# Optimization experiments

Hardware: AMD Instinct MI355X
Metric: run time of the kernel (lower is better)

## Reference

```python
import jax, jax.numpy as jnp
import numpy as np


def setup_inputs() -> dict:
    key = jax.random.key(0)
    ks = jax.random.split(key, 5)
    N, D, H, E = 8192, 1024, 4096, 8
    s = 0.02
    return {
        "x": jax.random.normal(ks[0], (N, D), jnp.float32),
        "Wr": jax.random.normal(ks[1], (D, E), jnp.float32) * s,
        "br": jnp.zeros((E,), jnp.float32),
        "W1": jax.random.normal(ks[2], (E, D, H), jnp.float32) * s,
        "b1": jnp.zeros((E, H), jnp.float32),
        "W2": jax.random.normal(ks[3], (E, H, D), jnp.float32) * s,
        "b2": jnp.zeros((E, D), jnp.float32),
        "k": 2,
    }


def reference(x, Wr, br, W1, b1, W2, b2, k):
    # Router (eval mode: no gate noise)
    logits = x @ Wr + br                      # [N, E]
    scores = jax.nn.softmax(logits, axis=-1)  # [N, E]
    topk_vals, topk_inds = jax.lax.top_k(scores, k)  # [N, k]
    N, E = scores.shape
    # dispatch_mask: zeros scattered with top-k probabilities
    dispatch_mask = jnp.zeros_like(scores).at[
        jnp.arange(N)[:, None], topk_inds
    ].set(topk_vals)                          # [N, E]
    # Dense all-expert FFN compute (faithful to the original wasteful pattern)
    h = jax.nn.relu(jnp.einsum('nd,edh->neh', x, W1) + b1)   # [N, E, H]
    expert_outputs = jnp.einsum('neh,ehd->ned', h, W2) + b2  # [N, E, D]
    output = jnp.einsum('ned,ne->nd', expert_outputs, dispatch_mask)  # [N, D]
    # Load-balancing aux loss (torch.var is unbiased, ddof=1)
    importance = dispatch_mask.sum(axis=0)    # [E]
    imp_mean = jnp.mean(importance)
    imp_var = jnp.var(importance, ddof=1)
    aux_loss = imp_var / (imp_mean ** 2 + 1e-9)
    return output, aux_loss
```

## Files before the change

### kernel.cpp

```cpp
#include <hip/hip_runtime.h>
#include <hip/hip_bf16.h>


#define NTOK 8192
#define DDIM 1024
#define HDIM 4096
#define NEXP 8
#define NASSIGN (NTOK * 2)
#define MAX_MT 72

typedef __bf16 bf16_t;
typedef __bf16 bf16x8 __attribute__((ext_vector_type(8)));
typedef float f32x4 __attribute__((ext_vector_type(4)));

#define GLOAD16(gptr, lptr)                                                    \
  __builtin_amdgcn_global_load_lds(                                            \
      (const __attribute__((address_space(1))) void*)(gptr),                   \
      (__attribute__((address_space(3))) void*)(lptr), 16, 0, 0)


__global__ void __launch_bounds__(256) cvt_x_kernel(
    const float* __restrict__ in, bf16_t* __restrict__ out) {
  const int i = (blockIdx.x * 256 + threadIdx.x) * 8;
  const float4 a = *(const float4*)(in + i);
  const float4 b = *(const float4*)(in + i + 4);
  bf16x8 o;
  o[0] = (bf16_t)a.x; o[1] = (bf16_t)a.y; o[2] = (bf16_t)a.z; o[3] = (bf16_t)a.w;
  o[4] = (bf16_t)b.x; o[5] = (bf16_t)b.y; o[6] = (bf16_t)b.z; o[7] = (bf16_t)b.w;
  *(bf16x8*)(out + i) = o;
}

__global__ void __launch_bounds__(256) transpose_cvt_kernel(
    const float* __restrict__ in, bf16_t* __restrict__ out, int R, int C) {
  __shared__ float tile[32][33];
  const size_t mat = (size_t)R * C;
  const float* ip = in + (size_t)blockIdx.z * mat;
  bf16_t* op = out + (size_t)blockIdx.z * mat;
  const int c0 = blockIdx.x * 32, r0 = blockIdx.y * 32;
  const int tx = threadIdx.x, ty = threadIdx.y;
#pragma unroll
  for (int i = 0; i < 4; ++i) {
    const int r = ty + 8 * i;
    tile[r][tx] = ip[(size_t)(r0 + r) * C + (c0 + tx)];
  }
  __syncthreads();
#pragma unroll
  for (int i = 0; i < 4; ++i) {
    const int r = ty + 8 * i;
    op[(size_t)(c0 + r) * R + (r0 + tx)] = (bf16_t)tile[tx][r];
  }
}


__global__ void __launch_bounds__(256) router_kernel(
    const float* __restrict__ x, const float* __restrict__ Wr,
    const float* __restrict__ br, int2* __restrict__ ids,
    float2* __restrict__ prs, int* __restrict__ counts) {
  const int n = blockIdx.x;
  const int t = threadIdx.x;
  const float* xr = x + (size_t)n * DDIM;
  float acc[NEXP];
#pragma unroll
  for (int e = 0; e < NEXP; ++e) acc[e] = 0.f;
#pragma unroll
  for (int j = 0; j < DDIM / 256; ++j) {
    const int d = t + 256 * j;
    const float xv = xr[d];
    const float* w = Wr + (size_t)d * NEXP;
#pragma unroll
    for (int e = 0; e < NEXP; ++e) acc[e] += xv * w[e];
  }
  __shared__ float red[256][NEXP];
#pragma unroll
  for (int e = 0; e < NEXP; ++e) red[t][e] = acc[e];
  __syncthreads();
  for (int s = 128; s >= 1; s >>= 1) {
    if (t < s) {
#pragma unroll
      for (int e = 0; e < NEXP; ++e) red[t][e] += red[t + s][e];
    }
    __syncthreads();
  }
  if (t == 0) {
    float l[NEXP];
#pragma unroll
    for (int e = 0; e < NEXP; ++e) l[e] = red[0][e] + br[e];
    int i1 = 0; float v1 = l[0];
    for (int e = 1; e < NEXP; ++e)
      if (l[e] > v1) { v1 = l[e]; i1 = e; }
    int i2 = (i1 == 0) ? 1 : 0; float v2 = l[i2];
    for (int e = 0; e < NEXP; ++e)
      if (e != i1 && l[e] > v2) { v2 = l[e]; i2 = e; }
    float denom = 0.f;
    for (int e = 0; e < NEXP; ++e) denom += expf(l[e] - v1);
    const float p1 = expf(v1 - v1) / denom;
    const float p2 = expf(v2 - v1) / denom;
    ids[n] = make_int2(i1, i2);
    prs[n] = make_float2(p1, p2);
    atomicAdd(&counts[i1], 1);
    atomicAdd(&counts[i2], 1);
  }
}

__global__ void __launch_bounds__(256) scan_aux_kernel(
    const int* __restrict__ counts, int* __restrict__ offsets,
    int* __restrict__ tmap, const int2* __restrict__ ids,
    const float2* __restrict__ prs, float* __restrict__ aux_out) {
  const int t = threadIdx.x;
  if (t == 0) {
    int off = 0, nt = 0;
    for (int e = 0; e < NEXP; ++e) {
      offsets[e] = off;
      const int c = counts[e];
      for (int m0 = 0; m0 < c; m0 += 256) {
        tmap[nt] = e;
        tmap[MAX_MT + nt] = m0;
        ++nt;
      }
      off += c;
    }
    offsets[NEXP] = off;
    tmap[2 * MAX_MT] = nt;
  }
  float imp[NEXP];
#pragma unroll
  for (int e = 0; e < NEXP; ++e) imp[e] = 0.f;
  for (int n = t; n < NTOK; n += 256) {
    const int2 id = ids[n];
    const float2 pr = prs[n];
#pragma unroll
    for (int e = 0; e < NEXP; ++e)
      imp[e] += (id.x == e ? pr.x : 0.f) + (id.y == e ? pr.y : 0.f);
  }
  __shared__ float red[256][NEXP];
#pragma unroll
  for (int e = 0; e < NEXP; ++e) red[t][e] = imp[e];
  __syncthreads();
  for (int s = 128; s >= 1; s >>= 1) {
    if (t < s) {
#pragma unroll
      for (int e = 0; e < NEXP; ++e) red[t][e] += red[t + s][e];
    }
    __syncthreads();
  }
  if (t == 0) {
    float m = 0.f;
    for (int e = 0; e < NEXP; ++e) m += red[0][e];
    m *= (1.f / NEXP);
    float v = 0.f;
    for (int e = 0; e < NEXP; ++e) {
      const float d = red[0][e] - m;
      v += d * d;
    }
    v *= (1.f / (NEXP - 1));
    aux_out[0] = v / (m * m + 1e-9f);
  }
}

__global__ void __launch_bounds__(256) scatter_kernel(
    const int2* __restrict__ ids, const float2* __restrict__ prs,
    const int* __restrict__ offsets, int* __restrict__ cursor,
    int* __restrict__ btok, float* __restrict__ bprob) {
  const int n = blockIdx.x * 256 + threadIdx.x;
  if (n >= NTOK) return;
  const int2 id = ids[n];
  const float2 pr = prs[n];
  int p = atomicAdd(&cursor[id.x], 1);
  btok[offsets[id.x] + p] = n;
  bprob[offsets[id.x] + p] = pr.x;
  p = atomicAdd(&cursor[id.y], 1);
  btok[offsets[id.y] + p] = n;
  bprob[offsets[id.y] + p] = pr.y;
}


__global__ void __launch_bounds__(512, 2) gemm1_kernel(
    const bf16_t* __restrict__ xb, const bf16_t* __restrict__ W1t,
    const float* __restrict__ b1, const int* __restrict__ btok,
    const int* __restrict__ offsets, const int* __restrict__ counts,
    const int* __restrict__ tmap, bf16_t* __restrict__ h) {
  const int tidx = blockIdx.y;
  if (tidx >= tmap[2 * MAX_MT]) return;
  const int e = tmap[tidx];
  const int m0 = tmap[MAX_MT + tidx];
  const int cnt = counts[e];
  const int aoff = offsets[e];
  const int n0 = blockIdx.x * 256;

  __shared__ __align__(16) bf16_t Al[256 * 32];
  __shared__ __align__(16) bf16_t Bl[256 * 32];

  const int tid = threadIdx.x;
  const int wave = tid >> 6;
  const int lane = tid & 63;

  const bf16_t* asrc[2];
  const bf16_t* bsrc[2];
#pragma unroll
  for (int j = 0; j < 2; ++j) {
    const int c = j * 512 + tid;
    const int r = c >> 2;
    const int kc = (c & 3) * 8;
    int arow = m0 + r;
    if (arow > cnt - 1) arow = cnt - 1;
    const int tok = btok[aoff + arow];
    asrc[j] = xb + (size_t)tok * DDIM + kc;
    bsrc[j] = W1t + ((size_t)e * HDIM + n0 + r) * DDIM + kc;
  }
  char* AlB = (char*)Al + wave * 1024;
  char* BlB = (char*)Bl + wave * 1024;

  f32x4 acc[8][4];
#pragma unroll
  for (int mf = 0; mf < 8; ++mf)
#pragma unroll
    for (int nf = 0; nf < 4; ++nf) acc[mf][nf] = (f32x4){0.f, 0.f, 0.f, 0.f};

  const int wr = (wave >> 2) * 128;
  const int wc = (wave & 3) * 64;
  const int lrow = lane & 15;
  const int lk = (lane >> 4) * 8;

  for (int k0 = 0; k0 < DDIM; k0 += 32) {
    GLOAD16(asrc[0] + k0, AlB);
    GLOAD16(asrc[1] + k0, AlB + 8192);
    GLOAD16(bsrc[0] + k0, BlB);
    GLOAD16(bsrc[1] + k0, BlB + 8192);
    __syncthreads();
    bf16x8 af[8], bfr[4];
#pragma unroll
    for (int mf = 0; mf < 8; ++mf)
      af[mf] = *(const bf16x8*)&Al[(wr + mf * 16 + lrow) * 32 + lk];
#pragma unroll
    for (int nf = 0; nf < 4; ++nf)
      bfr[nf] = *(const bf16x8*)&Bl[(wc + nf * 16 + lrow) * 32 + lk];
#pragma unroll
    for (int mf = 0; mf < 8; ++mf)
#pragma unroll
      for (int nf = 0; nf < 4; ++nf)
        acc[mf][nf] = __builtin_amdgcn_mfma_f32_16x16x32_bf16(
            af[mf], bfr[nf], acc[mf][nf], 0, 0, 0);
    __syncthreads();
  }

  const int rbase = (lane >> 4) * 4;
  const float* b1e = b1 + (size_t)e * HDIM + n0;
#pragma unroll
  for (int nf = 0; nf < 4; ++nf) {
    const int cl = wc + nf * 16 + lrow;
    const float bb = b1e[cl];
#pragma unroll
    for (int mf = 0; mf < 8; ++mf) {
#pragma unroll
      for (int r = 0; r < 4; ++r) {
        const int grow = wr + mf * 16 + rbase + r;
        if (m0 + grow < cnt)
          h[(size_t)(aoff + m0 + grow) * HDIM + (n0 + cl)] =
              (bf16_t)fmaxf(acc[mf][nf][r] + bb, 0.f);
      }
    }
  }
}

__global__ void __launch_bounds__(512, 2) gemm2_kernel(
    const bf16_t* __restrict__ h, const bf16_t* __restrict__ W2t,
    const float* __restrict__ b2, const int* __restrict__ btok,
    const float* __restrict__ bprob, const int* __restrict__ offsets,
    const int* __restrict__ counts, const int* __restrict__ tmap,
    float* __restrict__ out) {
  const int tidx = blockIdx.y;
  if (tidx >= tmap[2 * MAX_MT]) return;
  const int e = tmap[tidx];
  const int m0 = tmap[MAX_MT + tidx];
  const int cnt = counts[e];
  const int aoff = offsets[e];
  const int n0 = blockIdx.x * 256;

  __shared__ __align__(16) bf16_t Al[256 * 32];
  __shared__ __align__(16) bf16_t Bl[256 * 32];

  const int tid = threadIdx.x;
  const int wave = tid >> 6;
  const int lane = tid & 63;

  const bf16_t* asrc[2];
  const bf16_t* bsrc[2];
#pragma unroll
  for (int j = 0; j < 2; ++j) {
    const int c = j * 512 + tid;
    const int r = c >> 2;
    const int kc = (c & 3) * 8;
    int arow = m0 + r;
    if (arow > cnt - 1) arow = cnt - 1;
    asrc[j] = h + (size_t)(aoff + arow) * HDIM + kc;
    bsrc[j] = W2t + ((size_t)e * DDIM + n0 + r) * HDIM + kc;
  }
  char* AlB = (char*)Al + wave * 1024;
  char* BlB = (char*)Bl + wave * 1024;

  f32x4 acc[8][4];
#pragma unroll
  for (int mf = 0; mf < 8; ++mf)
#pragma unroll
    for (int nf = 0; nf < 4; ++nf) acc[mf][nf] = (f32x4){0.f, 0.f, 0.f, 0.f};

  const int wr = (wave >> 2) * 128;
  const int wc = (wave & 3) * 64;
  const int lrow = lane & 15;
  const int lk = (lane >> 4) * 8;

  for (int k0 = 0; k0 < HDIM; k0 += 32) {
    GLOAD16(asrc[0] + k0, AlB);
    GLOAD16(asrc[1] + k0, AlB + 8192);
    GLOAD16(bsrc[0] + k0, BlB);
    GLOAD16(bsrc[1] + k0, BlB + 8192);
    __syncthreads();
    bf16x8 af[8], bfr[4];
#pragma unroll
    for (int mf = 0; mf < 8; ++mf)
      af[mf] = *(const bf16x8*)&Al[(wr + mf * 16 + lrow) * 32 + lk];
#pragma unroll
    for (int nf = 0; nf < 4; ++nf)
      bfr[nf] = *(const bf16x8*)&Bl[(wc + nf * 16 + lrow) * 32 + lk];
#pragma unroll
    for (int mf = 0; mf < 8; ++mf)
#pragma unroll
      for (int nf = 0; nf < 4; ++nf)
        acc[mf][nf] = __builtin_amdgcn_mfma_f32_16x16x32_bf16(
            af[mf], bfr[nf], acc[mf][nf], 0, 0, 0);
    __syncthreads();
  }

  const int rbase = (lane >> 4) * 4;
  const float* b2e = b2 + (size_t)e * DDIM + n0;
  float bb[4];
#pragma unroll
  for (int nf = 0; nf < 4; ++nf) bb[nf] = b2e[wc + nf * 16 + lrow];
#pragma unroll
  for (int mf = 0; mf < 8; ++mf) {
#pragma unroll
    for (int r = 0; r < 4; ++r) {
      const int grow = wr + mf * 16 + rbase + r;
      if (m0 + grow < cnt) {
        const int assign = aoff + m0 + grow;
        const int tok = btok[assign];
        const float p = bprob[assign];
        float* orow = out + (size_t)tok * DDIM + n0;
#pragma unroll
        for (int nf = 0; nf < 4; ++nf) {
          const int cl = wc + nf * 16 + lrow;
          atomicAdd(&orow[cl], (acc[mf][nf][r] + bb[nf]) * p);
        }
      }
    }
  }
}


extern "C" void kernel_launch(void* const* d_in, const int* in_sizes, int n_in,
                              void* d_out, int out_size, void* d_ws,
                              size_t ws_size, hipStream_t stream) {
  const float* x = (const float*)d_in[0];
  const float* Wr = (const float*)d_in[1];
  const float* br = (const float*)d_in[2];
  const float* W1 = (const float*)d_in[3];
  const float* b1 = (const float*)d_in[4];
  const float* W2 = (const float*)d_in[5];
  const float* b2 = (const float*)d_in[6];

  char* w = (char*)d_ws;
  auto alloc = [&](size_t bytes) -> char* {
    char* p = w;
    w += (bytes + 255) & ~(size_t)255;
    return p;
  };
  bf16_t* xb = (bf16_t*)alloc((size_t)NTOK * DDIM * 2);
  bf16_t* W1t = (bf16_t*)alloc((size_t)NEXP * DDIM * HDIM * 2);
  bf16_t* W2t = (bf16_t*)alloc((size_t)NEXP * DDIM * HDIM * 2);
  bf16_t* hbuf = (bf16_t*)alloc((size_t)NASSIGN * HDIM * 2);
  int* btok = (int*)alloc(NASSIGN * 4);
  float* bprob = (float*)alloc(NASSIGN * 4);
  int2* ids = (int2*)alloc(NTOK * 8);
  float2* prs = (float2*)alloc(NTOK * 8);
  int* ctrl = (int*)alloc(64);
  int* offsets = (int*)alloc(64);
  int* tmap = (int*)alloc((2 * MAX_MT + 1) * 4);
  int* counts = ctrl;
  int* cursor = ctrl + 8;
  (void)in_sizes; (void)n_in; (void)ws_size;

  float* out = (float*)d_out;

  hipMemsetAsync(d_out, 0, (size_t)out_size * 4, stream);
  hipMemsetAsync(ctrl, 0, 64, stream);

  cvt_x_kernel<<<NTOK * DDIM / 2048, 256, 0, stream>>>(x, xb);
  transpose_cvt_kernel<<<dim3(HDIM / 32, DDIM / 32, NEXP), dim3(32, 8), 0,
                         stream>>>(W1, W1t, DDIM, HDIM);
  transpose_cvt_kernel<<<dim3(DDIM / 32, HDIM / 32, NEXP), dim3(32, 8), 0,
                         stream>>>(W2, W2t, HDIM, DDIM);
  router_kernel<<<NTOK, 256, 0, stream>>>(x, Wr, br, ids, prs, counts);
  scan_aux_kernel<<<1, 256, 0, stream>>>(counts, offsets, tmap, ids, prs,
                                         out + (size_t)NTOK * DDIM);
  scatter_kernel<<<NTOK / 256, 256, 0, stream>>>(ids, prs, offsets, cursor,
                                                 btok, bprob);
  gemm1_kernel<<<dim3(HDIM / 256, MAX_MT, 1), 512, 0, stream>>>(
      xb, W1t, b1, btok, offsets, counts, tmap, hbuf);
  gemm2_kernel<<<dim3(DDIM / 256, MAX_MT, 1), 512, 0, stream>>>(
      hbuf, W2t, b2, btok, bprob, offsets, counts, tmap, out);
}
```

Baseline: 1.020 ms.

## Double-buffer expert GEMMs with BK=64, split-K gemm2, fuse x conversion into router

Both expert GEMM kernels now load 64-wide K tiles into two LDS buffers. The next tile is prefetched with global_load_lds while the current one feeds the MFMAs, and s_setprio raises priority around the MFMA section. gemm2 is split into 4 K-chunks over the grid so far more blocks run; it relies on the existing atomicAdd epilogue, with the bias added only by the first chunk. The separate x→bf16 conversion kernel is folded into the router, which already reads x. The cost is 128KB of LDS per block, which probably allows only one block per CU despite the launch bounds, plus 4× more atomic traffic into the output.

```diff
diff --git a/kernel.cpp b/kernel.cpp
--- a/kernel.cpp
+++ b/kernel.cpp
@@ -8,8 +8,10 @@
 #define NEXP 8
 #define NASSIGN (NTOK * 2)
 #define MAX_MT 72
+#define KSPLIT 4
 
 typedef __bf16 bf16_t;
+typedef __bf16 bf16x4 __attribute__((ext_vector_type(4)));
 typedef __bf16 bf16x8 __attribute__((ext_vector_type(8)));
 typedef float f32x4 __attribute__((ext_vector_type(4)));
 
@@ -18,17 +20,6 @@
       (const __attribute__((address_space(1))) void*)(gptr),                   \
       (__attribute__((address_space(3))) void*)(lptr), 16, 0, 0)
 
-
-__global__ void __launch_bounds__(256) cvt_x_kernel(
-    const float* __restrict__ in, bf16_t* __restrict__ out) {
-  const int i = (blockIdx.x * 256 + threadIdx.x) * 8;
-  const float4 a = *(const float4*)(in + i);
-  const float4 b = *(const float4*)(in + i + 4);
-  bf16x8 o;
-  o[0] = (bf16_t)a.x; o[1] = (bf16_t)a.y; o[2] = (bf16_t)a.z; o[3] = (bf16_t)a.w;
-  o[4] = (bf16_t)b.x; o[5] = (bf16_t)b.y; o[6] = (bf16_t)b.z; o[7] = (bf16_t)b.w;
-  *(bf16x8*)(out + i) = o;
-}
 
 __global__ void __launch_bounds__(256) transpose_cvt_kernel(
     const float* __restrict__ in, bf16_t* __restrict__ out, int R, int C) {
@@ -55,20 +46,25 @@
 __global__ void __launch_bounds__(256) router_kernel(
     const float* __restrict__ x, const float* __restrict__ Wr,
     const float* __restrict__ br, int2* __restrict__ ids,
-    float2* __restrict__ prs, int* __restrict__ counts) {
+    float2* __restrict__ prs, int* __restrict__ counts,
+    bf16_t* __restrict__ xb) {
   const int n = blockIdx.x;
   const int t = threadIdx.x;
-  const float* xr = x + (size_t)n * DDIM;
+  const float4 xv = ((const float4*)(x + (size_t)n * DDIM))[t];
+  bf16x4 o;
+  o[0] = (bf16_t)xv.x; o[1] = (bf16_t)xv.y;
+  o[2] = (bf16_t)xv.z; o[3] = (bf16_t)xv.w;
+  ((bf16x4*)(xb + (size_t)n * DDIM))[t] = o;
+
   float acc[NEXP];
 #pragma unroll
   for (int e = 0; e < NEXP; ++e) acc[e] = 0.f;
-#pragma unroll
-  for (int j = 0; j < DDIM / 256; ++j) {
-    const int d = t + 256 * j;
-    const float xv = xr[d];
-    const float* w = Wr + (size_t)d * NEXP;
-#pragma unroll
-    for (int e = 0; e < NEXP; ++e) acc[e] += xv * w[e];
+  const float xq[4] = {xv.x, xv.y, xv.z, xv.w};
+#pragma unroll
+  for (int q = 0; q < 4; ++q) {
+    const float* w = Wr + (size_t)(4 * t + q) * NEXP;
+#pragma unroll
+    for (int e = 0; e < NEXP; ++e) acc[e] += xq[q] * w[e];
   }
   __shared__ float red[256][NEXP];
 #pragma unroll
@@ -93,7 +89,7 @@
       if (e != i1 && l[e] > v2) { v2 = l[e]; i2 = e; }
     float denom = 0.f;
     for (int e = 0; e < NEXP; ++e) denom += expf(l[e] - v1);
-    const float p1 = expf(v1 - v1) / denom;
+    const float p1 = 1.f / denom;
     const float p2 = expf(v2 - v1) / denom;
     ids[n] = make_int2(i1, i2);
     prs[n] = make_float2(p1, p2);
@@ -187,28 +183,25 @@
   const int aoff = offsets[e];
   const int n0 = blockIdx.x * 256;
 
-  __shared__ __align__(16) bf16_t Al[256 * 32];
-  __shared__ __align__(16) bf16_t Bl[256 * 32];
+  __shared__ __align__(16) bf16_t Al[2][256 * 64];
+  __shared__ __align__(16) bf16_t Bl[2][256 * 64];
 
   const int tid = threadIdx.x;
   const int wave = tid >> 6;
   const int lane = tid & 63;
 
-  const bf16_t* asrc[2];
-  const bf16_t* bsrc[2];
-#pragma unroll
-  for (int j = 0; j < 2; ++j) {
+  const bf16_t* asrc[4];
+  const bf16_t* bsrc[4];
+#pragma unroll
+  for (int j = 0; j < 4; ++j) {
     const int c = j * 512 + tid;
-    const int r = c >> 2;
-    const int kc = (c & 3) * 8;
+    const int r = c >> 3;
+    const int kc = (c & 7) * 8;
     int arow = m0 + r;
     if (arow > cnt - 1) arow = cnt - 1;
-    const int tok = btok[aoff + arow];
-    asrc[j] = xb + (size_t)tok * DDIM + kc;
+    asrc[j] = xb + (size_t)btok[aoff + arow] * DDIM + kc;
     bsrc[j] = W1t + ((size_t)e * HDIM + n0 + r) * DDIM + kc;
   }
-  char* AlB = (char*)Al + wave * 1024;
-  char* BlB = (char*)Bl + wave * 1024;
 
   f32x4 acc[8][4];
 #pragma unroll
@@ -219,27 +212,50 @@
   const int wr = (wave >> 2) * 128;
   const int wc = (wave & 3) * 64;
   const int lrow = lane & 15;
-  const int lk = (lane >> 4) * 8;
-
-  for (int k0 = 0; k0 < DDIM; k0 += 32) {
-    GLOAD16(asrc[0] + k0, AlB);
-    GLOAD16(asrc[1] + k0, AlB + 8192);
-    GLOAD16(bsrc[0] + k0, BlB);
-    GLOAD16(bsrc[1] + k0, BlB + 8192);
-    __syncthreads();
-    bf16x8 af[8], bfr[4];
-#pragma unroll
-    for (int mf = 0; mf < 8; ++mf)
-      af[mf] = *(const bf16x8*)&Al[(wr + mf * 16 + lrow) * 32 + lk];
-#pragma unroll
-    for (int nf = 0; nf < 4; ++nf)
-      bfr[nf] = *(const bf16x8*)&Bl[(wc + nf * 16 + lrow) * 32 + lk];
-#pragma unroll
-    for (int mf = 0; mf < 8; ++mf)
+  const int lk8 = (lane >> 4) * 8;
+
+  auto stage = [&](int b, int t) {
+    const int ko = t * 64;
+    char* Ab = (char*)&Al[b][0] + wave * 1024;
+    char* Bb = (char*)&Bl[b][0] + wave * 1024;
+#pragma unroll
+    for (int j = 0; j < 4; ++j) {
+      GLOAD16(asrc[j] + ko, Ab + j * 8192);
+      GLOAD16(bsrc[j] + ko, Bb + j * 8192);
+    }
+  };
+  auto compute = [&](int b) {
+    const bf16_t* Ab = &Al[b][0];
+    const bf16_t* Bb = &Bl[b][0];
+    __builtin_amdgcn_s_setprio(1);
+#pragma unroll
+    for (int ks = 0; ks < 2; ++ks) {
+      bf16x8 af[8], bfr[4];
+#pragma unroll
+      for (int mf = 0; mf < 8; ++mf)
+        af[mf] = *(const bf16x8*)&Ab[(wr + mf * 16 + lrow) * 64 + ks * 32 + lk8];
 #pragma unroll
       for (int nf = 0; nf < 4; ++nf)
-        acc[mf][nf] = __builtin_amdgcn_mfma_f32_16x16x32_bf16(
-            af[mf], bfr[nf], acc[mf][nf], 0, 0, 0);
+        bfr[nf] = *(const bf16x8*)&Bb[(wc + nf * 16 + lrow) * 64 + ks * 32 + lk8];
+#pragma unroll
+      for (int mf = 0; mf < 8; ++mf)
+#pragma unroll
+        for (int nf = 0; nf < 4; ++nf)
+          acc[mf][nf] = __builtin_amdgcn_mfma_f32_16x16x32_bf16(
+              af[mf], bfr[nf], acc[mf][nf], 0, 0, 0);
+    }
+    __builtin_amdgcn_s_setprio(0);
+  };
+
+  stage(0, 0);
+  __syncthreads();
+#pragma unroll
+  for (int t = 0; t < 16; t += 2) {
+    stage(1, t + 1);
+    compute(0);
+    __syncthreads();
+    if (t + 2 < 16) stage(0, t + 2);
+    compute(1);
     __syncthreads();
   }
 
@@ -268,7 +284,8 @@
     const float* __restrict__ bprob, const int* __restrict__ offsets,
     const int* __restrict__ counts, const int* __restrict__ tmap,
     float* __restrict__ out) {
-  const int tidx = blockIdx.y;
+  const int tidx = blockIdx.y >> 2;
+  const int kch = blockIdx.y & 3;
   if (tidx >= tmap[2 * MAX_MT]) return;
   const int e = tmap[tidx];
   const int m0 = tmap[MAX_MT + tidx];
@@ -276,27 +293,25 @@
   const int aoff = offsets[e];
   const int n0 = blockIdx.x * 256;
 
-  __shared__ __align__(16) bf16_t Al[256 * 32];
-  __shared__ __align__(16) bf16_t Bl[256 * 32];
+  __shared__ __align__(16) bf16_t Al[2][256 * 64];
+  __shared__ __align__(16) bf16_t Bl[2][256 * 64];
 
   const int tid = threadIdx.x;
   const int wave = tid >> 6;
   const int lane = tid & 63;
 
-  const bf16_t* asrc[2];
-  const bf16_t* bsrc[2];
-#pragma unroll
-  for (int j = 0; j < 2; ++j) {
+  const bf16_t* asrc[4];
+  const bf16_t* bsrc[4];
+#pragma unroll
+  for (int j = 0; j < 4; ++j) {
     const int c = j * 512 + tid;
-    const int r = c >> 2;
-    const int kc = (c & 3) * 8;
+    const int r = c >> 3;
+    const int kc = (c & 7) * 8 + kch * 1024;
     int arow = m0 + r;
     if (arow > cnt - 1) arow = cnt - 1;
     asrc[j] = h + (size_t)(aoff + arow) * HDIM + kc;
     bsrc[j] = W2t + ((size_t)e * DDIM + n0 + r) * HDIM + kc;
   }
-  char* AlB = (char*)Al + wave * 1024;
-  char* BlB = (char*)Bl + wave * 1024;
 
   f32x4 acc[8][4];
 #pragma unroll
@@ -307,27 +322,50 @@
   const int wr = (wave >> 2) * 128;
   const int wc = (wave & 3) * 64;
   const int lrow = lane & 15;
-  const int lk = (lane >> 4) * 8;
-
-  for (int k0 = 0; k0 < HDIM; k0 += 32) {
-    GLOAD16(asrc[0] + k0, AlB);
-    GLOAD16(asrc[1] + k0, AlB + 8192);
-    GLOAD16(bsrc[0] + k0, BlB);
-    GLOAD16(bsrc[1] + k0, BlB + 8192);
-    __syncthreads();
-    bf16x8 af[8], bfr[4];
-#pragma unroll
-    for (int mf = 0; mf < 8; ++mf)
-      af[mf] = *(const bf16x8*)&Al[(wr + mf * 16 + lrow) * 32 + lk];
-#pragma unroll
-    for (int nf = 0; nf < 4; ++nf)
-      bfr[nf] = *(const bf16x8*)&Bl[(wc + nf * 16 + lrow) * 32 + lk];
-#pragma unroll
-    for (int mf = 0; mf < 8; ++mf)
+  const int lk8 = (lane >> 4) * 8;
+
+  auto stage = [&](int b, int t) {
+    const int ko = t * 64;
+    char* Ab = (char*)&Al[b][0] + wave * 1024;
+    char* Bb = (char*)&Bl[b][0] + wave * 1024;
+#pragma unroll
+    for (int j = 0; j < 4; ++j) {
+      GLOAD16(asrc[j] + ko, Ab + j * 8192);
+      GLOAD16(bsrc[j] + ko, Bb + j * 8192);
+    }
+  };
+  auto compute = [&](int b) {
+    const bf16_t* Ab = &Al[b][0];
+    const bf16_t* Bb = &Bl[b][0];
+    __builtin_amdgcn_s_setprio(1);
+#pragma unroll
+    for (int ks = 0; ks < 2; ++ks) {
+      bf16x8 af[8], bfr[4];
+#pragma unroll
+      for (int mf = 0; mf < 8; ++mf)
+        af[mf] = *(const bf16x8*)&Ab[(wr + mf * 16 + lrow) * 64 + ks * 32 + lk8];
 #pragma unroll
       for (int nf = 0; nf < 4; ++nf)
-        acc[mf][nf] = __builtin_amdgcn_mfma_f32_16x16x32_bf16(
-            af[mf], bfr[nf], acc[mf][nf], 0, 0, 0);
+        bfr[nf] = *(const bf16x8*)&Bb[(wc + nf * 16 + lrow) * 64 + ks * 32 + lk8];
+#pragma unroll
+      for (int mf = 0; mf < 8; ++mf)
+#pragma unroll
+        for (int nf = 0; nf < 4; ++nf)
+          acc[mf][nf] = __builtin_amdgcn_mfma_f32_16x16x32_bf16(
+              af[mf], bfr[nf], acc[mf][nf], 0, 0, 0);
+    }
+    __builtin_amdgcn_s_setprio(0);
+  };
+
+  stage(0, 0);
+  __syncthreads();
+#pragma unroll
+  for (int t = 0; t < 16; t += 2) {
+    stage(1, t + 1);
+    compute(0);
+    __syncthreads();
+    if (t + 2 < 16) stage(0, t + 2);
+    compute(1);
     __syncthreads();
   }
 
@@ -335,7 +373,8 @@
   const float* b2e = b2 + (size_t)e * DDIM + n0;
   float bb[4];
 #pragma unroll
-  for (int nf = 0; nf < 4; ++nf) bb[nf] = b2e[wc + nf * 16 + lrow];
+  for (int nf = 0; nf < 4; ++nf)
+    bb[nf] = (kch == 0) ? b2e[wc + nf * 16 + lrow] : 0.f;
 #pragma unroll
   for (int mf = 0; mf < 8; ++mf) {
 #pragma unroll
@@ -394,18 +433,17 @@
   hipMemsetAsync(d_out, 0, (size_t)out_size * 4, stream);
   hipMemsetAsync(ctrl, 0, 64, stream);
 
-  cvt_x_kernel<<<NTOK * DDIM / 2048, 256, 0, stream>>>(x, xb);
   transpose_cvt_kernel<<<dim3(HDIM / 32, DDIM / 32, NEXP), dim3(32, 8), 0,
                          stream>>>(W1, W1t, DDIM, HDIM);
   transpose_cvt_kernel<<<dim3(DDIM / 32, HDIM / 32, NEXP), dim3(32, 8), 0,
                          stream>>>(W2, W2t, HDIM, DDIM);
-  router_kernel<<<NTOK, 256, 0, stream>>>(x, Wr, br, ids, prs, counts);
+  router_kernel<<<NTOK, 256, 0, stream>>>(x, Wr, br, ids, prs, counts, xb);
   scan_aux_kernel<<<1, 256, 0, stream>>>(counts, offsets, tmap, ids, prs,
                                          out + (size_t)NTOK * DDIM);
   scatter_kernel<<<NTOK / 256, 256, 0, stream>>>(ids, prs, offsets, cursor,
                                                  btok, bprob);
   gemm1_kernel<<<dim3(HDIM / 256, MAX_MT, 1), 512, 0, stream>>>(
       xb, W1t, b1, btok, offsets, counts, tmap, hbuf);
-  gemm2_kernel<<<dim3(DDIM / 256, MAX_MT, 1), 512, 0, stream>>>(
+  gemm2_kernel<<<dim3(DDIM / 256, MAX_MT * KSPLIT, 1), 512, 0, stream>>>(
       hbuf, W2t, b2, btok, bprob, offsets, counts, tmap, out);
 }
```

Measured after the change: 1.015 ms. About the same (-0.5%).
